# Performance work log

Hardware: AMD Instinct MI355X
Metric: run time of the kernel (lower is better)

Reference implementation:

```python
import jax, jax.numpy as jnp
import numpy as np

EPS = 1e-5

def maxpool2(x):
    # 2x2 max pool, stride 2, NCHW
    B, C, H, W = x.shape
    return x.reshape(B, C, H // 2, 2, W // 2, 2).max(axis=(3, 5))

def conv1x1(x, w, b):
    # x: [B,C,H,W], w: [O,C], b: [O]
    return jnp.einsum('bchw,oc->bohw', x, w) + b[None, :, None, None]

def setup_inputs() -> dict:
    key = jax.random.key(0)
    ks = jax.random.split(key, 12)
    B, C, IC, H, W = 8, 256, 128, 128, 128
    s = 0.05
    return {
        'rgb': jax.random.normal(ks[0], (B, C, H, W), jnp.float32),
        'event': jax.random.normal(ks[1], (B, C, H, W), jnp.float32),
        'g_w': jax.random.normal(ks[2], (IC, C), jnp.float32) * s,
        'g_b': jax.random.normal(ks[3], (IC,), jnp.float32) * s,
        'theta_w': jax.random.normal(ks[4], (IC, C), jnp.float32) * s,
        'theta_b': jax.random.normal(ks[5], (IC,), jnp.float32) * s,
        'phi_w': jax.random.normal(ks[6], (IC, C), jnp.float32) * s,
        'phi_b': jax.random.normal(ks[7], (IC,), jnp.float32) * s,
        'W_w': jax.random.normal(ks[8], (C, IC), jnp.float32) * s,
        'W_b': jax.random.normal(ks[9], (C,), jnp.float32) * s,
        'bn_gamma': jax.random.normal(ks[10], (C,), jnp.float32) * s + 1.0,
        'bn_beta': jax.random.normal(ks[11], (C,), jnp.float32) * s,
    }

def reference(rgb, event, g_w, g_b, theta_w, theta_b, phi_w, phi_b, W_w, W_b, bn_gamma, bn_beta):
    B = rgb.shape[0]
    IC = g_w.shape[0]
    # initial shared 2x2 max pool on both modalities
    rgb_p = maxpool2(rgb)      # [B,C,h2,w2]
    ev_p = maxpool2(event)
    h2, w2 = rgb_p.shape[2], rgb_p.shape[3]
    # projections; g and phi have an extra sub_sample pool
    g_x = maxpool2(conv1x1(ev_p, g_w, g_b)).reshape(B, IC, -1)      # [B,IC,Nkv]
    g_x = jnp.swapaxes(g_x, 1, 2)                                    # [B,Nkv,IC]
    theta_x = conv1x1(rgb_p, theta_w, theta_b).reshape(B, IC, -1)    # [B,IC,Nq]
    theta_x = jnp.swapaxes(theta_x, 1, 2)                            # [B,Nq,IC]
    phi_x = maxpool2(conv1x1(ev_p, phi_w, phi_b)).reshape(B, IC, -1) # [B,IC,Nkv]
    # full attention: scores -> softmax -> value matmul
    f = jnp.einsum('bqc,bck->bqk', theta_x, phi_x)                   # [B,Nq,Nkv]
    f_div_C = jax.nn.softmax(f, axis=-1)
    y = jnp.einsum('bqk,bkc->bqc', f_div_C, g_x)                     # [B,Nq,IC]
    y = jnp.swapaxes(y, 1, 2).reshape(B, IC, h2, w2)
    # output 1x1 conv + BatchNorm (training-mode batch stats, biased var)
    W_y = conv1x1(y, W_w, W_b)                                       # [B,C,h2,w2]
    mean = W_y.mean(axis=(0, 2, 3), keepdims=True)
    var = W_y.var(axis=(0, 2, 3), keepdims=True)
    W_y = (W_y - mean) * jax.lax.rsqrt(var + EPS)
    W_y = W_y * bn_gamma[None, :, None, None] + bn_beta[None, :, None, None]
    z = W_y + rgb_p
    z = jnp.repeat(jnp.repeat(z, 2, axis=2), 2, axis=3)
    return z
```

## Files before the change

kernel.cpp:

```cpp
#include <hip/hip_runtime.h>
#include <stdint.h>


typedef unsigned short u16;
typedef short bf16x8 __attribute__((ext_vector_type(8)));
typedef float f32x4 __attribute__((ext_vector_type(4)));

#define MFMA16(a, b, c) __builtin_amdgcn_mfma_f32_16x16x32_bf16(a, b, c, 0, 0, 0)

__device__ __forceinline__ u16 f2bf(float x) {
    union { float f; unsigned int u; } v; v.f = x;
    unsigned int u = v.u;
    unsigned int r = u + 0x7fffu + ((u >> 16) & 1u);
    return (u16)(r >> 16);
}
__device__ __forceinline__ float bf2f(u16 h) {
    union { unsigned int u; float f; } v; v.u = ((unsigned int)h) << 16;
    return v.f;
}

__global__ void zero_kernel(float* __restrict__ p, int n) {
    int i = blockIdx.x * 256 + threadIdx.x;
    if (i < n) p[i] = 0.0f;
}

__global__ void wsplit_kernel(const float* __restrict__ tw, const float* __restrict__ pw,
                              const float* __restrict__ gw, const float* __restrict__ ww,
                              u16* __restrict__ planes) {
    int idx = blockIdx.x * 256 + threadIdx.x;
    int m = idx >> 15, p = idx & 32767;
    const float* src = (m == 0) ? tw : (m == 1) ? pw : (m == 2) ? gw : ww;
    int se;
    if (m < 3) {
        int e = p & 7, lane = (p >> 3) & 63, kc = (p >> 9) & 7, ocb = p >> 12;
        int l16 = lane & 15, quad = lane >> 4;
        se = (ocb * 16 + l16) * 256 + kc * 32 + quad * 8 + e;
    } else {
        se = p;
    }
    float v = src[se];
    u16 h = f2bf(v);
    planes[m * 65536 + p] = h;
    planes[m * 65536 + 32768 + p] = f2bf(v - bf2f(h));
}

template <bool GCONV, bool POOLOUT>
__global__ __launch_bounds__(512) void fused_pool_conv_kernel(
    const float* __restrict__ x,
    const u16* __restrict__ W1h, const u16* __restrict__ W1l,
    const float* __restrict__ b1,
    const u16* __restrict__ W2h, const float* __restrict__ b2,
    u16* __restrict__ o1_hi, u16* __restrict__ o1_lo, u16* __restrict__ o2,
    u16* __restrict__ pool_hi) {
    __shared__ u16 Ph[64 * 256];
    __shared__ u16 Plo[64 * 256];

    int bx = blockIdx.x;
    int b = bx >> 6, h2 = bx & 63;
    int tid = threadIdx.x;
    int lane = tid & 63, quad = lane >> 4, l16 = lane & 15;
    int w = tid >> 6, mhalf = w & 1, nq = w >> 1;

    bf16x8 wh[2][2], wl[2][2], wg[2][2];
#pragma unroll
    for (int nt = 0; nt < 2; nt++) {
        long wo = ((long)((nq * 2 + nt) * 8 + 0) * 64 + lane) * 8;
        wh[0][nt] = *(const bf16x8*)&W1h[wo];
        wl[0][nt] = *(const bf16x8*)&W1l[wo];
        if (GCONV) wg[0][nt] = *(const bf16x8*)&W2h[wo];
    }

    long ibase = (long)b * 256 * 16384 + (long)(2 * h2) * 128;
#pragma unroll 8
    for (int i = 0; i < 16; i++) {
        int u = i * 512 + tid;
        int c = u >> 5, w4 = u & 31;
        const float* p = &x[ibase + (long)c * 16384 + w4 * 4];
        float4 r0 = *(const float4*)p;
        float4 r1 = *(const float4*)(p + 128);
        float p0 = fmaxf(fmaxf(r0.x, r0.y), fmaxf(r1.x, r1.y));
        float p1 = fmaxf(fmaxf(r0.z, r0.w), fmaxf(r1.z, r1.w));
        int row0 = 2 * w4, row1 = row0 + 1;
        int g = c >> 3, e = c & 7;
        u16 h0 = f2bf(p0), l0 = f2bf(p0 - bf2f(h0));
        u16 h1 = f2bf(p1), l1 = f2bf(p1 - bf2f(h1));
        int o0 = row0 * 256 + (((g ^ (row0 & 31)) << 3) | e);
        int o1 = row1 * 256 + (((g ^ (row1 & 31)) << 3) | e);
        Ph[o0] = h0; Plo[o0] = l0;
        Ph[o1] = h1; Plo[o1] = l1;
    }
    __syncthreads();

    f32x4 a1[2][2];
    f32x4 a2[GCONV ? 2 : 1][2];
#pragma unroll
    for (int mt = 0; mt < 2; mt++)
#pragma unroll
        for (int nt = 0; nt < 2; nt++) {
#pragma unroll
            for (int r = 0; r < 4; r++) a1[mt][nt][r] = 0.0f;
            if (GCONV)
#pragma unroll
                for (int r = 0; r < 4; r++) a2[mt][nt][r] = 0.0f;
        }

#pragma unroll
    for (int kc = 0; kc < 8; kc++) {
        int cur = kc & 1, nxt = cur ^ 1;
        if (kc < 7) {
#pragma unroll
            for (int nt = 0; nt < 2; nt++) {
                long wo = ((long)((nq * 2 + nt) * 8 + (kc + 1)) * 64 + lane) * 8;
                wh[nxt][nt] = *(const bf16x8*)&W1h[wo];
                wl[nxt][nt] = *(const bf16x8*)&W1l[wo];
                if (GCONV) wg[nxt][nt] = *(const bf16x8*)&W2h[wo];
            }
        }
        bf16x8 ah[2], al[2];
#pragma unroll
        for (int mt = 0; mt < 2; mt++) {
            int arow = mhalf * 32 + mt * 16 + l16;
            int g = kc * 4 + quad;
            int off = arow * 256 + ((g ^ (arow & 31)) << 3);
            ah[mt] = *(const bf16x8*)&Ph[off];
            al[mt] = *(const bf16x8*)&Plo[off];
        }
#pragma unroll
        for (int mt = 0; mt < 2; mt++)
#pragma unroll
            for (int nt = 0; nt < 2; nt++) {
                a1[mt][nt] = MFMA16(ah[mt], wh[cur][nt], a1[mt][nt]);
                a1[mt][nt] = MFMA16(ah[mt], wl[cur][nt], a1[mt][nt]);
                a1[mt][nt] = MFMA16(al[mt], wh[cur][nt], a1[mt][nt]);
                if (GCONV) a2[mt][nt] = MFMA16(ah[mt], wg[cur][nt], a2[mt][nt]);
            }
    }

    long mbase = (long)b * 4096 + h2 * 64;
#pragma unroll
    for (int mt = 0; mt < 2; mt++)
#pragma unroll
        for (int nt = 0; nt < 2; nt++) {
            int colo = nq * 32 + nt * 16 + l16;
            float bv1 = b1[colo];
            float bv2 = GCONV ? b2[colo] : 0.0f;
#pragma unroll
            for (int r = 0; r < 4; r++) {
                long row = mbase + mhalf * 32 + mt * 16 + quad * 4 + r;
                long idx = row * 128 + colo;
                float v = a1[mt][nt][r] + bv1;
                u16 h = f2bf(v);
                o1_hi[idx] = h;
                o1_lo[idx] = f2bf(v - bf2f(h));
                if (GCONV) o2[idx] = f2bf(a2[mt][nt][r] + bv2);
            }
        }

    if (POOLOUT) {
#pragma unroll 4
        for (int i = 0; i < 16; i++) {
            int r = i * 4 + (tid >> 7);
            int c = (tid & 127) * 2;
            int g = c >> 3;
            ushort2 hh = *(const ushort2*)&Ph[r * 256 + (((g ^ (r & 31)) << 3) | (c & 7))];
            *(ushort2*)&pool_hi[(mbase + r) * 256 + c] = hh;
        }
    }
}

__global__ __launch_bounds__(256) void pool_phiK_kernel(
    const u16* __restrict__ fhi, const u16* __restrict__ flo,
    u16* __restrict__ khi, u16* __restrict__ klo) {
    int idx = blockIdx.x * 256 + threadIdx.x;
    int c8 = (idx & 15) * 8;
    int kv = (idx >> 4) & 1023;
    int b = idx >> 14;
    int h4 = kv >> 5, w4 = kv & 31;
    long p00 = ((long)b * 4096 + (2 * h4) * 64 + 2 * w4) * 128 + c8;
    bf16x8 h0 = *(const bf16x8*)&fhi[p00];
    bf16x8 h1 = *(const bf16x8*)&fhi[p00 + 128];
    bf16x8 h2 = *(const bf16x8*)&fhi[p00 + 8192];
    bf16x8 h3 = *(const bf16x8*)&fhi[p00 + 8320];
    bf16x8 l0 = *(const bf16x8*)&flo[p00];
    bf16x8 l1 = *(const bf16x8*)&flo[p00 + 128];
    bf16x8 l2 = *(const bf16x8*)&flo[p00 + 8192];
    bf16x8 l3 = *(const bf16x8*)&flo[p00 + 8320];
    bf16x8 oh, ol;
#pragma unroll
    for (int e = 0; e < 8; e++) {
        float v = fmaxf(fmaxf(bf2f((u16)h0[e]) + bf2f((u16)l0[e]),
                              bf2f((u16)h1[e]) + bf2f((u16)l1[e])),
                        fmaxf(bf2f((u16)h2[e]) + bf2f((u16)l2[e]),
                              bf2f((u16)h3[e]) + bf2f((u16)l3[e])));
        u16 h = f2bf(v);
        oh[e] = (short)h;
        ol[e] = (short)f2bf(v - bf2f(h));
    }
    long oi = ((long)b * 1024 + kv) * 128 + c8;
    *(bf16x8*)&khi[oi] = oh;
    *(bf16x8*)&klo[oi] = ol;
}

__global__ __launch_bounds__(256) void pool_gVt_kernel(
    const u16* __restrict__ g, u16* __restrict__ vt) {
    __shared__ u16 t[64][65];
    int bx = blockIdx.x;
    int ct = bx & 1, kvt = (bx >> 1) & 15, b = bx >> 5;
    int tid = threadIdx.x;
#pragma unroll 4
    for (int i = 0; i < 16; i++) {
        int idx = i * 256 + tid;
        int kv_l = idx >> 6, c_l = idx & 63;
        int kv = kvt * 64 + kv_l;
        int h4 = kv >> 5, w4 = kv & 31;
        long p00 = ((long)b * 4096 + (2 * h4) * 64 + 2 * w4) * 128 + ct * 64 + c_l;
        float v = fmaxf(fmaxf(bf2f(g[p00]), bf2f(g[p00 + 128])),
                        fmaxf(bf2f(g[p00 + 8192]), bf2f(g[p00 + 8192 + 128])));
        t[c_l][kv_l] = f2bf(v);
    }
    __syncthreads();
    long ob = ((long)b * 128 + ct * 64) * 1024 + kvt * 64;
#pragma unroll 4
    for (int i = 0; i < 16; i++) {
        int idx = i * 256 + tid;
        int c_l = idx >> 6, kv_l = idx & 63;
        vt[ob + (long)c_l * 1024 + kv_l] = t[c_l][kv_l];
    }
}

__global__ __launch_bounds__(512, 4) void attn_kernel(
    const u16* __restrict__ th, const u16* __restrict__ tl,
    const u16* __restrict__ khi, const u16* __restrict__ klo,
    const u16* __restrict__ vt, u16* __restrict__ y) {
    __shared__ u16 Kh[2][32][136];
    __shared__ u16 Kl[2][32][136];
    __shared__ u16 Vt[2][128][40];
    __shared__ u16 Pl[8][16][40];

    int bx = blockIdx.x;
    int b = bx & 7, qt = bx >> 3;
    int tid = threadIdx.x;
    int w = tid >> 6, g = w >> 2, wsub = w & 3;
    int lane = tid & 63, quad = lane >> 4, l16 = lane & 15;
    int qbase = qt * 64 + wsub * 16;

    bf16x8 qh[4], ql[4];
    long tb = ((long)b * 4096 + qbase + l16) * 128;
#pragma unroll
    for (int kc = 0; kc < 4; kc++) {
        qh[kc] = *(const bf16x8*)&th[tb + kc * 32 + quad * 8];
        ql[kc] = *(const bf16x8*)&tl[tb + kc * 32 + quad * 8];
    }

    f32x4 o[8];
#pragma unroll
    for (int t2 = 0; t2 < 8; t2++)
#pragma unroll
        for (int r = 0; r < 4; r++) o[t2][r] = 0.0f;
    float lp[4] = {0.0f, 0.0f, 0.0f, 0.0f};

#pragma unroll 1
    for (int it = 0; it < 16; it++) {
        __syncthreads();
#pragma unroll
        for (int j = 0; j < 2; j++) {
            int c0 = j * 512 + tid;
            int row = (c0 >> 4) & 31, ko = (c0 & 15) * 8;
            long src = ((long)b * 1024 + j * 512 + it * 32 + row) * 128 + ko;
            *(uint4*)&Kh[j][row][ko] = *(const uint4*)&khi[src];
            *(uint4*)&Kl[j][row][ko] = *(const uint4*)&klo[src];
        }
#pragma unroll
        for (int j = 0; j < 2; j++) {
            int c0 = j * 512 + tid;
            int crow = (c0 >> 2) & 127, ko = (c0 & 3) * 8;
            long src = ((long)b * 128 + crow) * 1024 + j * 512 + it * 32 + ko;
            *(uint4*)&Vt[j][crow][ko] = *(const uint4*)&vt[src];
        }
        __syncthreads();

        f32x4 s[2];
#pragma unroll
        for (int nt = 0; nt < 2; nt++)
#pragma unroll
            for (int r = 0; r < 4; r++) s[nt][r] = 0.0f;
#pragma unroll
        for (int kc = 0; kc < 4; kc++) {
#pragma unroll
            for (int nt = 0; nt < 2; nt++) {
                bf16x8 bh = *(const bf16x8*)&Kh[g][nt * 16 + l16][kc * 32 + quad * 8];
                bf16x8 bl = *(const bf16x8*)&Kl[g][nt * 16 + l16][kc * 32 + quad * 8];
                s[nt] = MFMA16(qh[kc], bh, s[nt]);
                s[nt] = MFMA16(qh[kc], bl, s[nt]);
                s[nt] = MFMA16(ql[kc], bh, s[nt]);
            }
        }

#pragma unroll
        for (int nt = 0; nt < 2; nt++)
#pragma unroll
            for (int r = 0; r < 4; r++) {
                float p = __expf(s[nt][r]);
                lp[r] += p;
                Pl[w][quad * 4 + r][nt * 16 + l16] = f2bf(p);
            }

        bf16x8 pa = *(const bf16x8*)&Pl[w][l16][quad * 8];
#pragma unroll
        for (int t2 = 0; t2 < 8; t2++) {
            bf16x8 vb = *(const bf16x8*)&Vt[g][t2 * 16 + l16][quad * 8];
            o[t2] = MFMA16(pa, vb, o[t2]);
        }
    }

#pragma unroll
    for (int r = 0; r < 4; r++)
#pragma unroll
        for (int off = 1; off < 16; off <<= 1) lp[r] += __shfl_xor(lp[r], off);

    __syncthreads();
    float* Ob = (float*)&Kh[0][0][0];
    float* Lb = (float*)&Vt[0][0][0];
    if (g == 1) {
#pragma unroll
        for (int t2 = 0; t2 < 8; t2++)
#pragma unroll
            for (int r = 0; r < 4; r++)
                Ob[(wsub * 16 + quad * 4 + r) * 132 + t2 * 16 + l16] = o[t2][r];
        if (l16 == 0)
#pragma unroll
            for (int r = 0; r < 4; r++) Lb[wsub * 16 + quad * 4 + r] = lp[r];
    }
    __syncthreads();
    if (g == 0) {
#pragma unroll
        for (int r = 0; r < 4; r++) {
            int lrow = wsub * 16 + quad * 4 + r;
            float inv = 1.0f / (lp[r] + Lb[lrow]);
            long row = (long)b * 4096 + qbase + quad * 4 + r;
#pragma unroll
            for (int t2 = 0; t2 < 8; t2++) {
                float ov = o[t2][r] + Ob[lrow * 132 + t2 * 16 + l16];
                y[row * 128 + t2 * 16 + l16] = f2bf(ov * inv);
            }
        }
    }
}

__global__ __launch_bounds__(256) void wconv_kernel(
    const u16* __restrict__ A, const u16* __restrict__ Wh,
    const float* __restrict__ bias, float* __restrict__ out_f,
    float* __restrict__ acc_g) {
    __shared__ float red[4][2][256];
    int tid = threadIdx.x;
    int wave = tid >> 6, lane = tid & 63, quad = lane >> 4, l16 = lane & 15;
    long mbase = (long)blockIdx.x * 64 + wave * 16;

    f32x4 acc[16];
#pragma unroll
    for (int nt = 0; nt < 16; nt++)
#pragma unroll
        for (int r = 0; r < 4; r++) acc[nt][r] = 0.0f;

#pragma unroll
    for (int kc = 0; kc < 4; kc++) {
        bf16x8 ah = *(const bf16x8*)&A[(mbase + l16) * 128 + kc * 32 + quad * 8];
#pragma unroll
        for (int nt = 0; nt < 16; nt++) {
            bf16x8 bh = *(const bf16x8*)&Wh[(long)(nt * 16 + l16) * 128 + kc * 32 + quad * 8];
            acc[nt] = MFMA16(ah, bh, acc[nt]);
        }
    }

#pragma unroll
    for (int nt = 0; nt < 16; nt++) {
        int colo = nt * 16 + l16;
        float bv = bias[colo];
        float vs = 0.0f, vq = 0.0f;
#pragma unroll
        for (int r = 0; r < 4; r++) {
            long row = mbase + quad * 4 + r;
            float v = acc[nt][r] + bv;
            out_f[row * 256 + colo] = v;
            vs += v;
            vq += v * v;
        }
        vs += __shfl_xor(vs, 16); vs += __shfl_xor(vs, 32);
        vq += __shfl_xor(vq, 16); vq += __shfl_xor(vq, 32);
        if (quad == 0) {
            red[wave][0][colo] = vs;
            red[wave][1][colo] = vq;
        }
    }
    __syncthreads();
    if (tid < 256) {
        int c = tid;
        float s = red[0][0][c] + red[1][0][c] + red[2][0][c] + red[3][0][c];
        float q = red[0][1][c] + red[1][1][c] + red[2][1][c] + red[3][1][c];
        atomicAdd(&acc_g[c], s);
        atomicAdd(&acc_g[256 + c], q);
    }
}

__global__ __launch_bounds__(256) void final_kernel(
    const float* __restrict__ wy, const u16* __restrict__ rgbhi,
    const float* __restrict__ acc, const float* __restrict__ gamma,
    const float* __restrict__ beta, float* __restrict__ out) {
    __shared__ float z[16][257];
    int bx = blockIdx.x;
    int wt = bx & 3, h2 = (bx >> 2) & 63, b = bx >> 8;
    int c = threadIdx.x;

    float mean = acc[c] * (1.0f / 32768.0f);
    float var = acc[256 + c] * (1.0f / 32768.0f) - mean * mean;
    float rstd = rsqrtf(var + 1e-5f);
    float gm = gamma[c] * rstd;
    float bt = beta[c] - mean * gm;

    long pbase = (long)b * 4096 + h2 * 64 + wt * 16;
#pragma unroll 4
    for (int i = 0; i < 16; i++) {
        long pi = (pbase + i) * 256 + c;
        z[i][c] = wy[pi] * gm + bt + bf2f(rgbhi[pi]);
    }
    __syncthreads();
    int tid = threadIdx.x;
#pragma unroll 4
    for (int pass = 0; pass < 64; pass++) {
        int cc = pass * 4 + (tid >> 6);
        int r = (tid >> 5) & 1, wc = tid & 31;
        float v = z[wc >> 1][cc];
        out[(((long)b * 256 + cc) * 128 + 2 * h2 + r) * 128 + wt * 32 + wc] = v;
    }
}

extern "C" void kernel_launch(void* const* d_in, const int* in_sizes, int n_in,
                              void* d_out, int out_size, void* d_ws, size_t ws_size,
                              hipStream_t stream) {
    const float* rgb     = (const float*)d_in[0];
    const float* event_  = (const float*)d_in[1];
    const float* g_w     = (const float*)d_in[2];
    const float* g_b     = (const float*)d_in[3];
    const float* theta_w = (const float*)d_in[4];
    const float* theta_b = (const float*)d_in[5];
    const float* phi_w   = (const float*)d_in[6];
    const float* phi_b   = (const float*)d_in[7];
    const float* W_w     = (const float*)d_in[8];
    const float* W_b     = (const float*)d_in[9];
    const float* gamma   = (const float*)d_in[10];
    const float* beta    = (const float*)d_in[11];

    char* ws = (char*)d_ws;
    u16* rgbpt_hi = (u16*)(ws + 0);
    u16* theta_hi = (u16*)(ws + 16777216);
    u16* theta_lo = (u16*)(ws + 25165824);
    u16* phiF_hi  = (u16*)(ws + 33554432);
    u16* phiF_lo  = (u16*)(ws + 41943040);
    u16* g_full   = (u16*)(ws + 50331648);
    u16* phiK_hi  = (u16*)(ws + 58720256);
    u16* phiK_lo  = (u16*)(ws + 60817408);
    u16* gVt      = (u16*)(ws + 62914560);
    u16* y        = (u16*)(ws + 65011712);
    float* Wy     = (float*)(ws + 73400320);
    u16* wplanes  = (u16*)(ws + 106954752);
    float* acc    = (float*)(ws + 107479040);

    zero_kernel<<<2, 256, 0, stream>>>(acc, 512);
    wsplit_kernel<<<512, 256, 0, stream>>>(theta_w, phi_w, g_w, W_w, wplanes);

    fused_pool_conv_kernel<false, true><<<512, 512, 0, stream>>>(
        rgb, wplanes + 0, wplanes + 32768, theta_b,
        nullptr, nullptr, theta_hi, theta_lo, nullptr, rgbpt_hi);
    fused_pool_conv_kernel<true, false><<<512, 512, 0, stream>>>(
        event_, wplanes + 65536, wplanes + 98304, phi_b,
        wplanes + 131072, g_b, phiF_hi, phiF_lo, g_full, nullptr);

    pool_phiK_kernel<<<512, 256, 0, stream>>>(phiF_hi, phiF_lo, phiK_hi, phiK_lo);
    pool_gVt_kernel<<<256, 256, 0, stream>>>(g_full, gVt);

    attn_kernel<<<512, 512, 0, stream>>>(theta_hi, theta_lo, phiK_hi, phiK_lo, gVt, y);

    wconv_kernel<<<512, 256, 0, stream>>>(y, wplanes + 196608, W_b, Wy, acc);

    final_kernel<<<2048, 256, 0, stream>>>(Wy, rgbpt_hi, acc, gamma, beta, (float*)d_out);
}
```

Before: 486.1 us.

## Merge launches, stagger channel reads, and prefetch attention K/V tiles into registers

```diff
diff --git a/kernel.cpp b/kernel.cpp
--- a/kernel.cpp
+++ b/kernel.cpp
@@ -19,14 +19,13 @@
     return v.f;
 }
 
-__global__ void zero_kernel(float* __restrict__ p, int n) {
-    int i = blockIdx.x * 256 + threadIdx.x;
-    if (i < n) p[i] = 0.0f;
-}
-
 __global__ void wsplit_kernel(const float* __restrict__ tw, const float* __restrict__ pw,
                               const float* __restrict__ gw, const float* __restrict__ ww,
-                              u16* __restrict__ planes) {
+                              u16* __restrict__ planes, float* __restrict__ acc) {
+    if (blockIdx.x == 0) {
+        acc[threadIdx.x] = 0.0f;
+        acc[256 + threadIdx.x] = 0.0f;
+    }
     int idx = blockIdx.x * 256 + threadIdx.x;
     int m = idx >> 15, p = idx & 32767;
     const float* src = (m == 0) ? tw : (m == 1) ? pw : (m == 2) ? gw : ww;
@@ -44,22 +43,31 @@
     planes[m * 65536 + 32768 + p] = f2bf(v - bf2f(h));
 }
 
-template <bool GCONV, bool POOLOUT>
 __global__ __launch_bounds__(512) void fused_pool_conv_kernel(
-    const float* __restrict__ x,
-    const u16* __restrict__ W1h, const u16* __restrict__ W1l,
-    const float* __restrict__ b1,
-    const u16* __restrict__ W2h, const float* __restrict__ b2,
-    u16* __restrict__ o1_hi, u16* __restrict__ o1_lo, u16* __restrict__ o2,
-    u16* __restrict__ pool_hi) {
+    const float* __restrict__ xr, const float* __restrict__ xe,
+    const u16* __restrict__ Th, const u16* __restrict__ Tl, const float* __restrict__ tb,
+    const u16* __restrict__ Fh, const u16* __restrict__ Fl, const float* __restrict__ fb,
+    const u16* __restrict__ Gh, const float* __restrict__ gb,
+    u16* __restrict__ th_o, u16* __restrict__ tl_o,
+    u16* __restrict__ fh_o, u16* __restrict__ fl_o,
+    u16* __restrict__ g_o, u16* __restrict__ pool_hi) {
     __shared__ u16 Ph[64 * 256];
     __shared__ u16 Plo[64 * 256];
 
     int bx = blockIdx.x;
-    int b = bx >> 6, h2 = bx & 63;
+    bool ev = bx >= 512;
+    int bxx = bx & 511;
+    int b = bxx >> 6, h2 = bxx & 63;
     int tid = threadIdx.x;
     int lane = tid & 63, quad = lane >> 4, l16 = lane & 15;
     int w = tid >> 6, mhalf = w & 1, nq = w >> 1;
+
+    const float* x = ev ? xe : xr;
+    const u16* W1h = ev ? Fh : Th;
+    const u16* W1l = ev ? Fl : Tl;
+    const float* b1 = ev ? fb : tb;
+    u16* o1_hi = ev ? fh_o : th_o;
+    u16* o1_lo = ev ? fl_o : tl_o;
 
     bf16x8 wh[2][2], wl[2][2], wg[2][2];
 #pragma unroll
@@ -67,14 +75,16 @@
         long wo = ((long)((nq * 2 + nt) * 8 + 0) * 64 + lane) * 8;
         wh[0][nt] = *(const bf16x8*)&W1h[wo];
         wl[0][nt] = *(const bf16x8*)&W1l[wo];
-        if (GCONV) wg[0][nt] = *(const bf16x8*)&W2h[wo];
+        if (ev) wg[0][nt] = *(const bf16x8*)&Gh[wo];
     }
 
     long ibase = (long)b * 256 * 16384 + (long)(2 * h2) * 128;
+    int coff = (bx * 37) & 255;
 #pragma unroll 8
     for (int i = 0; i < 16; i++) {
         int u = i * 512 + tid;
-        int c = u >> 5, w4 = u & 31;
+        int c0 = u >> 5, w4 = u & 31;
+        int c = (c0 + coff) & 255;
         const float* p = &x[ibase + (long)c * 16384 + w4 * 4];
         float4 r0 = *(const float4*)p;
         float4 r1 = *(const float4*)(p + 128);
@@ -92,16 +102,15 @@
     __syncthreads();
 
     f32x4 a1[2][2];
-    f32x4 a2[GCONV ? 2 : 1][2];
+    f32x4 a2[2][2];
 #pragma unroll
     for (int mt = 0; mt < 2; mt++)
 #pragma unroll
         for (int nt = 0; nt < 2; nt++) {
 #pragma unroll
             for (int r = 0; r < 4; r++) a1[mt][nt][r] = 0.0f;
-            if (GCONV)
-#pragma unroll
-                for (int r = 0; r < 4; r++) a2[mt][nt][r] = 0.0f;
+#pragma unroll
+            for (int r = 0; r < 4; r++) a2[mt][nt][r] = 0.0f;
         }
 
 #pragma unroll
@@ -113,7 +122,7 @@
                 long wo = ((long)((nq * 2 + nt) * 8 + (kc + 1)) * 64 + lane) * 8;
                 wh[nxt][nt] = *(const bf16x8*)&W1h[wo];
                 wl[nxt][nt] = *(const bf16x8*)&W1l[wo];
-                if (GCONV) wg[nxt][nt] = *(const bf16x8*)&W2h[wo];
+                if (ev) wg[nxt][nt] = *(const bf16x8*)&Gh[wo];
             }
         }
         bf16x8 ah[2], al[2];
@@ -132,7 +141,7 @@
                 a1[mt][nt] = MFMA16(ah[mt], wh[cur][nt], a1[mt][nt]);
                 a1[mt][nt] = MFMA16(ah[mt], wl[cur][nt], a1[mt][nt]);
                 a1[mt][nt] = MFMA16(al[mt], wh[cur][nt], a1[mt][nt]);
-                if (GCONV) a2[mt][nt] = MFMA16(ah[mt], wg[cur][nt], a2[mt][nt]);
+                if (ev) a2[mt][nt] = MFMA16(ah[mt], wg[cur][nt], a2[mt][nt]);
             }
     }
 
@@ -143,7 +152,7 @@
         for (int nt = 0; nt < 2; nt++) {
             int colo = nq * 32 + nt * 16 + l16;
             float bv1 = b1[colo];
-            float bv2 = GCONV ? b2[colo] : 0.0f;
+            float bv2 = ev ? gb[colo] : 0.0f;
 #pragma unroll
             for (int r = 0; r < 4; r++) {
                 long row = mbase + mhalf * 32 + mt * 16 + quad * 4 + r;
@@ -152,11 +161,11 @@
                 u16 h = f2bf(v);
                 o1_hi[idx] = h;
                 o1_lo[idx] = f2bf(v - bf2f(h));
-                if (GCONV) o2[idx] = f2bf(a2[mt][nt][r] + bv2);
+                if (ev) g_o[idx] = f2bf(a2[mt][nt][r] + bv2);
             }
         }
 
-    if (POOLOUT) {
+    if (!ev) {
 #pragma unroll 4
         for (int i = 0; i < 16; i++) {
             int r = i * 4 + (tid >> 7);
@@ -168,63 +177,64 @@
     }
 }
 
-__global__ __launch_bounds__(256) void pool_phiK_kernel(
+__global__ __launch_bounds__(256) void pool_mid_kernel(
     const u16* __restrict__ fhi, const u16* __restrict__ flo,
-    u16* __restrict__ khi, u16* __restrict__ klo) {
-    int idx = blockIdx.x * 256 + threadIdx.x;
-    int c8 = (idx & 15) * 8;
-    int kv = (idx >> 4) & 1023;
-    int b = idx >> 14;
-    int h4 = kv >> 5, w4 = kv & 31;
-    long p00 = ((long)b * 4096 + (2 * h4) * 64 + 2 * w4) * 128 + c8;
-    bf16x8 h0 = *(const bf16x8*)&fhi[p00];
-    bf16x8 h1 = *(const bf16x8*)&fhi[p00 + 128];
-    bf16x8 h2 = *(const bf16x8*)&fhi[p00 + 8192];
-    bf16x8 h3 = *(const bf16x8*)&fhi[p00 + 8320];
-    bf16x8 l0 = *(const bf16x8*)&flo[p00];
-    bf16x8 l1 = *(const bf16x8*)&flo[p00 + 128];
-    bf16x8 l2 = *(const bf16x8*)&flo[p00 + 8192];
-    bf16x8 l3 = *(const bf16x8*)&flo[p00 + 8320];
-    bf16x8 oh, ol;
-#pragma unroll
-    for (int e = 0; e < 8; e++) {
-        float v = fmaxf(fmaxf(bf2f((u16)h0[e]) + bf2f((u16)l0[e]),
-                              bf2f((u16)h1[e]) + bf2f((u16)l1[e])),
-                        fmaxf(bf2f((u16)h2[e]) + bf2f((u16)l2[e]),
-                              bf2f((u16)h3[e]) + bf2f((u16)l3[e])));
-        u16 h = f2bf(v);
-        oh[e] = (short)h;
-        ol[e] = (short)f2bf(v - bf2f(h));
-    }
-    long oi = ((long)b * 1024 + kv) * 128 + c8;
-    *(bf16x8*)&khi[oi] = oh;
-    *(bf16x8*)&klo[oi] = ol;
-}
-
-__global__ __launch_bounds__(256) void pool_gVt_kernel(
-    const u16* __restrict__ g, u16* __restrict__ vt) {
+    u16* __restrict__ khi, u16* __restrict__ klo,
+    const u16* __restrict__ gsrc, u16* __restrict__ vt) {
     __shared__ u16 t[64][65];
-    int bx = blockIdx.x;
-    int ct = bx & 1, kvt = (bx >> 1) & 15, b = bx >> 5;
+    int bX = blockIdx.x;
     int tid = threadIdx.x;
+    if (bX < 512) {
+        int idx = bX * 256 + tid;
+        int c8 = (idx & 15) * 8;
+        int kv = (idx >> 4) & 1023;
+        int b = idx >> 14;
+        int h4 = kv >> 5, w4 = kv & 31;
+        long p00 = ((long)b * 4096 + (2 * h4) * 64 + 2 * w4) * 128 + c8;
+        bf16x8 h0 = *(const bf16x8*)&fhi[p00];
+        bf16x8 h1 = *(const bf16x8*)&fhi[p00 + 128];
+        bf16x8 h2 = *(const bf16x8*)&fhi[p00 + 8192];
+        bf16x8 h3 = *(const bf16x8*)&fhi[p00 + 8320];
+        bf16x8 l0 = *(const bf16x8*)&flo[p00];
+        bf16x8 l1 = *(const bf16x8*)&flo[p00 + 128];
+        bf16x8 l2 = *(const bf16x8*)&flo[p00 + 8192];
+        bf16x8 l3 = *(const bf16x8*)&flo[p00 + 8320];
+        bf16x8 oh, ol;
+#pragma unroll
+        for (int e = 0; e < 8; e++) {
+            float v = fmaxf(fmaxf(bf2f((u16)h0[e]) + bf2f((u16)l0[e]),
+                                  bf2f((u16)h1[e]) + bf2f((u16)l1[e])),
+                            fmaxf(bf2f((u16)h2[e]) + bf2f((u16)l2[e]),
+                                  bf2f((u16)h3[e]) + bf2f((u16)l3[e])));
+            u16 h = f2bf(v);
+            oh[e] = (short)h;
+            ol[e] = (short)f2bf(v - bf2f(h));
+        }
+        long oi = ((long)b * 1024 + kv) * 128 + c8;
+        *(bf16x8*)&khi[oi] = oh;
+        *(bf16x8*)&klo[oi] = ol;
+    } else {
+        int bx = bX - 512;
+        int ct = bx & 1, kvt = (bx >> 1) & 15, b = bx >> 5;
 #pragma unroll 4
-    for (int i = 0; i < 16; i++) {
-        int idx = i * 256 + tid;
-        int kv_l = idx >> 6, c_l = idx & 63;
-        int kv = kvt * 64 + kv_l;
-        int h4 = kv >> 5, w4 = kv & 31;
-        long p00 = ((long)b * 4096 + (2 * h4) * 64 + 2 * w4) * 128 + ct * 64 + c_l;
-        float v = fmaxf(fmaxf(bf2f(g[p00]), bf2f(g[p00 + 128])),
-                        fmaxf(bf2f(g[p00 + 8192]), bf2f(g[p00 + 8192 + 128])));
-        t[c_l][kv_l] = f2bf(v);
-    }
-    __syncthreads();
-    long ob = ((long)b * 128 + ct * 64) * 1024 + kvt * 64;
+        for (int i = 0; i < 16; i++) {
+            int idx = i * 256 + tid;
+            int kv_l = idx >> 6, c_l = idx & 63;
+            int kv = kvt * 64 + kv_l;
+            int h4 = kv >> 5, w4 = kv & 31;
+            long p00 = ((long)b * 4096 + (2 * h4) * 64 + 2 * w4) * 128 + ct * 64 + c_l;
+            float v = fmaxf(fmaxf(bf2f(gsrc[p00]), bf2f(gsrc[p00 + 128])),
+                            fmaxf(bf2f(gsrc[p00 + 8192]), bf2f(gsrc[p00 + 8192 + 128])));
+            t[c_l][kv_l] = f2bf(v);
+        }
+        __syncthreads();
+        long ob = ((long)b * 128 + ct * 64) * 1024 + kvt * 64;
 #pragma unroll 4
-    for (int i = 0; i < 16; i++) {
-        int idx = i * 256 + tid;
-        int c_l = idx >> 6, kv_l = idx & 63;
-        vt[ob + (long)c_l * 1024 + kv_l] = t[c_l][kv_l];
+        for (int i = 0; i < 16; i++) {
+            int idx = i * 256 + tid;
+            int c_l = idx >> 6, kv_l = idx & 63;
+            vt[ob + (long)c_l * 1024 + kv_l] = t[c_l][kv_l];
+        }
     }
 }
 
@@ -244,6 +254,32 @@
     int lane = tid & 63, quad = lane >> 4, l16 = lane & 15;
     int qbase = qt * 64 + wsub * 16;
 
+    int krow = (tid >> 4) & 31, kko = (tid & 15) * 8;
+    int vrow = (tid >> 2) & 127, vko = (tid & 3) * 8;
+    long kb0 = ((long)b * 1024 + krow) * 128 + kko;
+    long vb0 = ((long)b * 128 + vrow) * 1024 + vko;
+    uint4 rkh0, rkh1, rkl0, rkl1, rv0, rv1;
+
+#define STAGE_LOAD(IT) do {                                   \
+        long k0 = kb0 + (long)(IT) * 4096;                    \
+        rkh0 = *(const uint4*)&khi[k0];                       \
+        rkl0 = *(const uint4*)&klo[k0];                       \
+        rkh1 = *(const uint4*)&khi[k0 + 65536];               \
+        rkl1 = *(const uint4*)&klo[k0 + 65536];               \
+        long v0 = vb0 + (IT) * 32;                            \
+        rv0 = *(const uint4*)&vt[v0];                         \
+        rv1 = *(const uint4*)&vt[v0 + 512];                   \
+    } while (0)
+
+#define STAGE_WRITE() do {                                    \
+        *(uint4*)&Kh[0][krow][kko] = rkh0;                    \
+        *(uint4*)&Kl[0][krow][kko] = rkl0;                    \
+        *(uint4*)&Kh[1][krow][kko] = rkh1;                    \
+        *(uint4*)&Kl[1][krow][kko] = rkl1;                    \
+        *(uint4*)&Vt[0][vrow][vko] = rv0;                     \
+        *(uint4*)&Vt[1][vrow][vko] = rv1;                     \
+    } while (0)
+
     bf16x8 qh[4], ql[4];
     long tb = ((long)b * 4096 + qbase + l16) * 128;
 #pragma unroll
@@ -259,26 +295,13 @@
         for (int r = 0; r < 4; r++) o[t2][r] = 0.0f;
     float lp[4] = {0.0f, 0.0f, 0.0f, 0.0f};
 
+    STAGE_LOAD(0);
+    STAGE_WRITE();
+    __syncthreads();
+    STAGE_LOAD(1);
+
 #pragma unroll 1
     for (int it = 0; it < 16; it++) {
-        __syncthreads();
-#pragma unroll
-        for (int j = 0; j < 2; j++) {
-            int c0 = j * 512 + tid;
-            int row = (c0 >> 4) & 31, ko = (c0 & 15) * 8;
-            long src = ((long)b * 1024 + j * 512 + it * 32 + row) * 128 + ko;
-            *(uint4*)&Kh[j][row][ko] = *(const uint4*)&khi[src];
-            *(uint4*)&Kl[j][row][ko] = *(const uint4*)&klo[src];
-        }
-#pragma unroll
-        for (int j = 0; j < 2; j++) {
-            int c0 = j * 512 + tid;
-            int crow = (c0 >> 2) & 127, ko = (c0 & 3) * 8;
-            long src = ((long)b * 128 + crow) * 1024 + j * 512 + it * 32 + ko;
-            *(uint4*)&Vt[j][crow][ko] = *(const uint4*)&vt[src];
-        }
-        __syncthreads();
-
         f32x4 s[2];
 #pragma unroll
         for (int nt = 0; nt < 2; nt++)
@@ -311,6 +334,13 @@
             bf16x8 vb = *(const bf16x8*)&Vt[g][t2 * 16 + l16][quad * 8];
             o[t2] = MFMA16(pa, vb, o[t2]);
         }
+
+        __syncthreads();
+        if (it < 15) {
+            STAGE_WRITE();
+            __syncthreads();
+            if (it < 14) STAGE_LOAD(it + 2);
+        }
     }
 
 #pragma unroll
@@ -345,6 +375,8 @@
             }
         }
     }
+#undef STAGE_LOAD
+#undef STAGE_WRITE
 }
 
 __global__ __launch_bounds__(256) void wconv_kernel(
@@ -465,18 +497,17 @@
     u16* wplanes  = (u16*)(ws + 106954752);
     float* acc    = (float*)(ws + 107479040);
 
-    zero_kernel<<<2, 256, 0, stream>>>(acc, 512);
-    wsplit_kernel<<<512, 256, 0, stream>>>(theta_w, phi_w, g_w, W_w, wplanes);
-
-    fused_pool_conv_kernel<false, true><<<512, 512, 0, stream>>>(
-        rgb, wplanes + 0, wplanes + 32768, theta_b,
-        nullptr, nullptr, theta_hi, theta_lo, nullptr, rgbpt_hi);
-    fused_pool_conv_kernel<true, false><<<512, 512, 0, stream>>>(
-        event_, wplanes + 65536, wplanes + 98304, phi_b,
-        wplanes + 131072, g_b, phiF_hi, phiF_lo, g_full, nullptr);
-
-    pool_phiK_kernel<<<512, 256, 0, stream>>>(phiF_hi, phiF_lo, phiK_hi, phiK_lo);
-    pool_gVt_kernel<<<256, 256, 0, stream>>>(g_full, gVt);
+    wsplit_kernel<<<512, 256, 0, stream>>>(theta_w, phi_w, g_w, W_w, wplanes, acc);
+
+    fused_pool_conv_kernel<<<1024, 512, 0, stream>>>(
+        rgb, event_,
+        wplanes + 0, wplanes + 32768, theta_b,
+        wplanes + 65536, wplanes + 98304, phi_b,
+        wplanes + 131072, g_b,
+        theta_hi, theta_lo, phiF_hi, phiF_lo, g_full, rgbpt_hi);
+
+    pool_mid_kernel<<<768, 256, 0, stream>>>(phiF_hi, phiF_lo, phiK_hi, phiK_lo,
+                                             g_full, gVt);
 
     attn_kernel<<<512, 512, 0, stream>>>(theta_hi, theta_lo, phiK_hi, phiK_lo, gVt, y);
 
```

Result: faster. 462.6 us (-4.8%).
